# Kernel optimization log

Hardware: AMD Instinct MI355X
Metric: run time of the kernel (lower is better)

## Reference

```python
import jax, jax.numpy as jnp
import numpy as np

B, N, E = 2, 50000, 800000
IN_CH, SP_CH, OUT_CH, EDGE_CH = 64, 16, 32, 1


def _xavier(k, shape):
    scale = (2.0 / (shape[0] + shape[1])) ** 0.5
    return jax.random.normal(k, shape, dtype=jnp.float32) * scale


def setup_inputs() -> dict:
    key = jax.random.key(0)
    ks = jax.random.split(key, 20)
    return {
        "X": jax.random.normal(ks[0], (B, N, IN_CH), dtype=jnp.float32),
        "edge_index0": jax.random.randint(ks[1], (2, E), 0, N),
        "edge_index1": jax.random.randint(ks[2], (2, E), 0, N),
        "edge_weight0": jax.random.uniform(ks[3], (E, EDGE_CH), dtype=jnp.float32),
        "edge_weight1": jax.random.uniform(ks[4], (E, EDGE_CH), dtype=jnp.float32),
        "res_n_id0": jnp.arange(N),
        "res_n_id1": jnp.arange(N),
        # conv1 params (in=IN_CH, out=SP_CH)
        "value1": _xavier(ks[5], (IN_CH, SP_CH)),
        "key1": _xavier(ks[6], (SP_CH, SP_CH)),
        "query1": _xavier(ks[7], (SP_CH, SP_CH)),
        "we1": _xavier(ks[8], (EDGE_CH, SP_CH)),
        "att_w1": _xavier(ks[9], (3 * SP_CH, 1)),
        "att_b1": jnp.zeros((1,), jnp.float32),
        "cat_w1": _xavier(ks[10], (2 * SP_CH, SP_CH)),
        "cat_b1": jnp.zeros((SP_CH,), jnp.float32),
        # conv2 params (in=SP_CH, out=OUT_CH)
        "value2": _xavier(ks[11], (SP_CH, OUT_CH)),
        "key2": _xavier(ks[12], (OUT_CH, OUT_CH)),
        "query2": _xavier(ks[13], (OUT_CH, OUT_CH)),
        "we2": _xavier(ks[14], (EDGE_CH, OUT_CH)),
        "att_w2": _xavier(ks[15], (3 * OUT_CH, 1)),
        "att_b2": jnp.zeros((1,), jnp.float32),
        "cat_w2": _xavier(ks[16], (2 * OUT_CH, OUT_CH)),
        "cat_b2": jnp.zeros((OUT_CH,), jnp.float32),
    }


def _egnn_conv(Xs, Xd, ei, ef, value, key_w, query_w, we, att_w, att_b, cat_w, cat_b):
    # Xs: [B,Ns,Cin] source nodes, Xd: [B,Nd,Cin] dest nodes, ei: [2,E], ef: [E,edge_ch]
    xs = Xs @ value                       # [B,Ns,C]
    xd = Xd @ value                       # [B,Nd,C]
    e = ef @ we                           # [E,C]
    xj = xs[:, ei[0]]                     # [B,E,C] source gather
    xi = xd[:, ei[1]]                     # [B,E,C] dest gather
    q = xj @ query_w                      # note: original code names are swapped; kept faithful
    k = xi @ key_w
    att_in = jnp.concatenate([k, q, jnp.broadcast_to(e, q.shape)], axis=-1)  # [B,E,3C]
    att = jax.nn.sigmoid(att_in @ att_w + att_b)      # [B,E,1]
    msg = att * xj * jax.nn.sigmoid(e)                # [B,E,C]
    aggr = jnp.zeros(xd.shape, xd.dtype).at[:, ei[1]].add(msg)  # scatter-add over dest
    upd = jnp.concatenate([xd, aggr], axis=-1) @ cat_w + cat_b  # [B,Nd,C]
    return xd + jax.nn.relu(upd)


def reference(X, edge_index0, edge_index1, edge_weight0, edge_weight1,
              res_n_id0, res_n_id1,
              value1, key1, query1, we1, att_w1, att_b1, cat_w1, cat_b1,
              value2, key2, query2, we2, att_w2, att_b2, cat_w2, cat_b2):
    X1 = _egnn_conv(X, X[:, res_n_id0], edge_index0, edge_weight0,
                    value1, key1, query1, we1, att_w1, att_b1, cat_w1, cat_b1)
    X1 = jax.nn.leaky_relu(X1)  # negative_slope 0.01, matches torch default
    X2 = _egnn_conv(X1, X1[:, res_n_id1], edge_index1, edge_weight1,
                    value2, key2, query2, we2, att_w2, att_b2, cat_w2, cat_b2)
    return X2
```

## Files before the change

kernel.cpp:

```cpp
#include <hip/hip_runtime.h>
#include <hip/hip_fp16.h>

#define BB   2
#define NN   50000
#define EE   800000
#define INCH 64
#define C1   16
#define C2   32
#define NB   (BB*NN)

#define W1S   6
#define W2S   5
#define NBK1  ((NN + 63) >> 6)
#define NBK2  ((NN + 31) >> 5)
#define NBKT  (NBK1 + NBK2)
#define EB    4096
#define TPB   1024
#define NEBLK ((2*EE + EB - 1) / EB)

#define OFF_XS1   0
#define OFF_XS2   (OFF_XS1 + NB*C1/2)
#define OFF_DOTK1 (OFF_XS2 + NB*C2/2)
#define OFF_DOTQ1 (OFF_DOTK1 + NB)
#define OFF_DOTK2 (OFF_DOTQ1 + NB)
#define OFF_DOTQ2 (OFF_DOTK2 + NB)
#define OFF_AG1   (OFF_DOTQ2 + NB)
#define OFF_AG2   (OFF_AG1 + NN*32)
#define OFF_BTOT  (OFF_AG2 + NN*64)
#define OFF_BBASE (OFF_BTOT + NBKT)
#define OFF_START (OFF_BBASE + NBKT)
#define OFF_DEG   (OFF_START + 2*NN)
#define OFF_SC    (OFF_DEG + 2*NN)
#define OFF_RECS2 (OFF_SC + 2)
#define OFF_REGION (OFF_RECS2 + 2*EE*2)
#define OFF_RECS   OFF_REGION
#define OFF_BCNT   (OFF_REGION + 2*EE*2)

__device__ __forceinline__ float sigmoidf(float x) {
    return 1.0f / (1.0f + __expf(-x));
}

__global__ void k_sc(const float* __restrict__ we1, const float* __restrict__ aw1,
                     const float* __restrict__ we2, const float* __restrict__ aw2,
                     float* __restrict__ sc) {
    if (threadIdx.x == 0) {
        float e = 0.f;
        for (int j = 0; j < C1; ++j) e += we1[j] * aw1[2*C1+j];
        sc[0] = e;
    }
    if (threadIdx.x == 1) {
        float e = 0.f;
        for (int j = 0; j < C2; ++j) e += we2[j] * aw2[2*C2+j];
        sc[1] = e;
    }
}

__global__ __launch_bounds__(TPB) void k_cnt(
        const int* __restrict__ ei0, const int* __restrict__ ei1,
        unsigned* __restrict__ blockCnt) {
    __shared__ unsigned h[NBKT];
    int tid = threadIdx.x;
    for (int i = tid; i < NBKT; i += TPB) h[i] = 0u;
    __syncthreads();
    int base = blockIdx.x * EB;
#pragma unroll
    for (int j = 0; j < EB/TPB; ++j) {
        int t = base + j*TPB + tid;
        if (t < 2*EE) {
            int bkt;
            if (t < EE) { int dst = ei0[EE + t];      bkt = dst >> W1S; }
            else        { int dst = ei1[EE + t - EE]; bkt = NBK1 + (dst >> W2S); }
            atomicAdd(&h[bkt], 1u);
        }
    }
    __syncthreads();
    unsigned* o = blockCnt + (size_t)blockIdx.x * NBKT;
    for (int i = tid; i < NBKT; i += TPB) o[i] = h[i];
}

__global__ __launch_bounds__(512) void k_scanBkt(
        unsigned* __restrict__ blockCnt, unsigned* __restrict__ bktTot) {
    __shared__ unsigned s[512];
    int tid = threadIdx.x;
    int bkt = blockIdx.x;
    unsigned v = (tid < NEBLK) ? blockCnt[(size_t)tid * NBKT + bkt] : 0u;
    s[tid] = v;
    __syncthreads();
    for (int o = 1; o < 512; o <<= 1) {
        unsigned t = (tid >= o) ? s[tid - o] : 0u;
        __syncthreads();
        s[tid] += t;
        __syncthreads();
    }
    if (tid < NEBLK) blockCnt[(size_t)tid * NBKT + bkt] = s[tid] - v;
    if (tid == 511) bktTot[bkt] = s[511];
}

__global__ __launch_bounds__(1024) void k_scanTot(
        const unsigned* __restrict__ bktTot, unsigned* __restrict__ bucketBase) {
    __shared__ unsigned s[1024];
    int tid = threadIdx.x;
    int base = tid * 3;
    unsigned a0 = (base + 0 < NBKT) ? bktTot[base + 0] : 0u;
    unsigned a1 = (base + 1 < NBKT) ? bktTot[base + 1] : 0u;
    unsigned a2 = (base + 2 < NBKT) ? bktTot[base + 2] : 0u;
    unsigned l = a0 + a1 + a2;
    s[tid] = l;
    __syncthreads();
    for (int o = 1; o < 1024; o <<= 1) {
        unsigned t = (tid >= o) ? s[tid - o] : 0u;
        __syncthreads();
        s[tid] += t;
        __syncthreads();
    }
    unsigned ex = s[tid] - l;
    if (base + 0 < NBKT) bucketBase[base + 0] = ex;
    if (base + 1 < NBKT) bucketBase[base + 1] = ex + a0;
    if (base + 2 < NBKT) bucketBase[base + 2] = ex + a0 + a1;
}

__global__ __launch_bounds__(TPB) void k_permute(
        const int* __restrict__ ei0, const int* __restrict__ ei1,
        const float* __restrict__ ew0, const float* __restrict__ ew1,
        const unsigned* __restrict__ blockOff, const unsigned* __restrict__ bucketBase,
        uint2* __restrict__ recs) {
    __shared__ unsigned off[NBKT];
    __shared__ unsigned cur[NBKT];
    int tid = threadIdx.x;
    const unsigned* bo = blockOff + (size_t)blockIdx.x * NBKT;
    for (int i = tid; i < NBKT; i += TPB) { off[i] = bo[i] + bucketBase[i]; cur[i] = 0u; }
    __syncthreads();
    int base = blockIdx.x * EB;
#pragma unroll
    for (int j = 0; j < EB/TPB; ++j) {
        int t = base + j*TPB + tid;
        if (t >= 2*EE) break;
        int bkt, dl, src; float ef;
        if (t < EE) {
            int dst = ei0[EE + t];
            bkt = dst >> W1S; dl = dst & 63;
            src = ei0[t]; ef = ew0[t];
        } else {
            int e = t - EE;
            int dst = ei1[EE + e];
            bkt = NBK1 + (dst >> W2S); dl = dst & 31;
            src = ei1[e]; ef = ew1[e];
        }
        unsigned pos = off[bkt] + atomicAdd(&cur[bkt], 1u);
        recs[pos] = make_uint2((unsigned)src | ((unsigned)dl << 16), __float_as_uint(ef));
    }
}

__global__ __launch_bounds__(256) void k_sortb(
        const uint2* __restrict__ recs, const unsigned* __restrict__ bktTot,
        const unsigned* __restrict__ bucketBase,
        uint2* __restrict__ recs2, unsigned* __restrict__ startA,
        unsigned* __restrict__ degA) {
    __shared__ unsigned h[64], sOff[64], cur[64];
    int tid = threadIdx.x;
    int bkt = blockIdx.x;
    int lay1 = (bkt < NBK1) ? 1 : 0;
    int ndl  = lay1 ? 64 : 32;
    int nodeBase = lay1 ? (bkt << W1S) : ((bkt - NBK1) << W2S);
    int layOff   = lay1 ? 0 : NN;
    if (tid < 64) h[tid] = 0u;
    __syncthreads();
    unsigned cnt = bktTot[bkt], base = bucketBase[bkt];
    for (unsigned i = tid; i < cnt; i += 256)
        atomicAdd(&h[recs[base + i].x >> 16], 1u);
    __syncthreads();
    if (tid == 0) {
        unsigned run = 0;
        for (int d = 0; d < ndl; ++d) { sOff[d] = run; run += h[d]; }
    }
    __syncthreads();
    if (tid < ndl) {
        cur[tid] = sOff[tid];
        int node = nodeBase + tid;
        if (node < NN) {
            startA[layOff + node] = base + sOff[tid];
            degA[layOff + node]   = h[tid];
        }
    }
    __syncthreads();
    for (unsigned i = tid; i < cnt; i += 256) {
        uint2 r = recs[base + i];
        unsigned dl  = r.x >> 16;
        unsigned src = r.x & 0xffffu;
        unsigned pos = atomicAdd(&cur[dl], 1u);
        unsigned dst = (unsigned)nodeBase + dl;
        recs2[base + pos] = make_uint2(src | (dst << 16), r.y);
    }
}

__global__ __launch_bounds__(256) void k_value1(
        const float* __restrict__ X, const float* __restrict__ value1,
        const float* __restrict__ key1, const float* __restrict__ query1,
        const float* __restrict__ aw1,
        __half* __restrict__ xs1h, float* __restrict__ dotk1, float* __restrict__ dotq1) {
    __shared__ float W[INCH*C1];
    __shared__ float KV[C1], QV[C1];
    int tid = threadIdx.x;
    for (int i = tid; i < INCH*C1; i += 256) W[i] = value1[i];
    if (tid < C1) {
        float kv = 0.f, qv = 0.f;
#pragma unroll
        for (int j = 0; j < C1; ++j) {
            kv += key1[tid*C1+j]   * aw1[j];
            qv += query1[tid*C1+j] * aw1[C1+j];
        }
        KV[tid] = kv; QV[tid] = qv;
    }
    __syncthreads();
    int bn = blockIdx.x * 256 + tid;
    if (bn >= NB) return;
    int b = (bn >= NN) ? 1 : 0;
    int node = bn - b*NN;
    const float4* Xr = (const float4*)(X + (size_t)bn * INCH);
    float acc[C1];
#pragma unroll
    for (int j = 0; j < C1; ++j) acc[j] = 0.f;
#pragma unroll
    for (int v = 0; v < 16; ++v) {
        float4 p = Xr[v];
        float x4[4] = {p.x, p.y, p.z, p.w};
#pragma unroll
        for (int h = 0; h < 4; ++h) {
            int i = v*4 + h;
            float xv = x4[h];
#pragma unroll
            for (int j = 0; j < C1; ++j) acc[j] += xv * W[i*C1+j];
        }
    }
    float dk = 0.f, dq = 0.f;
#pragma unroll
    for (int j = 0; j < C1; ++j) { dk += acc[j]*KV[j]; dq += acc[j]*QV[j]; }
    __half* o = xs1h + ((size_t)node * C1) * 2 + b;
#pragma unroll
    for (int j = 0; j < C1; ++j) o[2*j] = __float2half_rn(acc[j]);
    dotk1[node*2 + b] = dk; dotq1[node*2 + b] = dq;
}

__global__ __launch_bounds__(256) void k_gath1(
        const uint2* __restrict__ recs2, const float* __restrict__ we,
        const float* __restrict__ ab, const float* __restrict__ sc,
        const uint2* __restrict__ xsh, const float* __restrict__ dotk,
        const float* __restrict__ dotq, uint2* __restrict__ msg) {
    int t = blockIdx.x * 256 + threadIdx.x;
    int p = t >> 3, cp = t & 7;
    uint2 rec = recs2[p];
    int src = rec.x & 0xffff, dst = rec.x >> 16;
    float ef = __uint_as_float(rec.y);
    float se0 = sigmoidf(ef * we[2*cp]);
    float se1 = sigmoidf(ef * we[2*cp+1]);
    float eb  = ef * sc[0] + ab[0];
    float2 dq = *(const float2*)(dotq + src*2);
    float2 dk = *(const float2*)(dotk + dst*2);
    float a0 = sigmoidf(dk.x + dq.x + eb);
    float a1 = sigmoidf(dk.y + dq.y + eb);
    uint2 xr = xsh[(size_t)src*8 + cp];
    float2 f0 = __half22float2(__builtin_bit_cast(__half2, xr.x));
    float2 f1 = __half22float2(__builtin_bit_cast(__half2, xr.y));
    __half2 m0 = __floats2half2_rn(a0*se0*f0.x, a1*se0*f0.y);
    __half2 m1 = __floats2half2_rn(a0*se1*f1.x, a1*se1*f1.y);
    msg[(size_t)p*8 + cp] = make_uint2(__builtin_bit_cast(unsigned, m0),
                                       __builtin_bit_cast(unsigned, m1));
}

__global__ __launch_bounds__(256) void k_red1(
        const unsigned* __restrict__ startA, const unsigned* __restrict__ degA,
        const uint2* __restrict__ msg, float* __restrict__ aggrf) {
    int t = blockIdx.x * 256 + threadIdx.x;
    int node = t >> 3, cp = t & 7;
    if (node >= NN) return;
    unsigned s = startA[node];
    unsigned n = degA[node];
    float a0 = 0.f, a1 = 0.f, a2 = 0.f, a3 = 0.f;
    const uint2* mp = msg + (size_t)s*8 + cp;
    for (unsigned i = 0; i < n; ++i) {
        uint2 v = mp[(size_t)i*8];
        float2 f0 = __half22float2(__builtin_bit_cast(__half2, v.x));
        float2 f1 = __half22float2(__builtin_bit_cast(__half2, v.y));
        a0 += f0.x; a1 += f0.y; a2 += f1.x; a3 += f1.y;
    }
    ((float4*)aggrf)[(size_t)node*8 + cp] = make_float4(a0, a1, a2, a3);
}

__global__ __launch_bounds__(256) void k_update1(
        const float* __restrict__ cat_w, const float* __restrict__ cat_b,
        const float* __restrict__ value2,
        const float* __restrict__ key2, const float* __restrict__ query2,
        const float* __restrict__ aw2,
        const __half* __restrict__ xs1h, const float* __restrict__ aggr1f,
        __half* __restrict__ xs2h, float* __restrict__ dotk2, float* __restrict__ dotq2) {
    __shared__ float CW[2*C1*C1];
    __shared__ float CB[C1];
    __shared__ float V2[C1*C2];
    __shared__ float KV[C2], QV[C2];
    int tid = threadIdx.x;
    for (int i = tid; i < 2*C1*C1; i += 256) CW[i] = cat_w[i];
    for (int i = tid; i < C1*C2;   i += 256) V2[i] = value2[i];
    if (tid < C1) CB[tid] = cat_b[tid];
    if (tid < C2) {
        float kv = 0.f;
#pragma unroll
        for (int j = 0; j < C2; ++j) kv += key2[tid*C2+j] * aw2[j];
        KV[tid] = kv;
    } else if (tid < 2*C2) {
        int c = tid - C2;
        float qv = 0.f;
#pragma unroll
        for (int j = 0; j < C2; ++j) qv += query2[c*C2+j] * aw2[C2+j];
        QV[c] = qv;
    }
    __syncthreads();
    int bn = blockIdx.x * 256 + tid;
    if (bn >= NB) return;
    int b = (bn >= NN) ? 1 : 0;
    int node = bn - b*NN;
    const __half* xr = xs1h + ((size_t)node*C1)*2 + b;
    const float* agp = aggr1f + (size_t)node*32;
    float xd[C1], ag[C1];
#pragma unroll
    for (int i = 0; i < C1; ++i) xd[i] = __half2float(xr[2*i]);
#pragma unroll
    for (int i = 0; i < C1; ++i) ag[i] = agp[(i>>1)*4 + (i&1)*2 + b];
    float x1[C1];
#pragma unroll
    for (int j = 0; j < C1; ++j) {
        float u = CB[j];
#pragma unroll
        for (int i = 0; i < C1; ++i) {
            u += xd[i] * CW[i*C1 + j];
            u += ag[i] * CW[(C1+i)*C1 + j];
        }
        float o = xd[j] + fmaxf(u, 0.f);
        x1[j] = (o > 0.f) ? o : 0.01f * o;
    }
    float o2[C2];
#pragma unroll
    for (int k = 0; k < C2; ++k) o2[k] = 0.f;
#pragma unroll
    for (int j = 0; j < C1; ++j) {
        float xv = x1[j];
#pragma unroll
        for (int k = 0; k < C2; ++k) o2[k] += xv * V2[j*C2 + k];
    }
    float dk = 0.f, dq = 0.f;
#pragma unroll
    for (int k = 0; k < C2; ++k) { dk += o2[k]*KV[k]; dq += o2[k]*QV[k]; }
    __half* o = xs2h + ((size_t)node*C2)*2 + b;
#pragma unroll
    for (int k = 0; k < C2; ++k) o[2*k] = __float2half_rn(o2[k]);
    dotk2[node*2 + b] = dk; dotq2[node*2 + b] = dq;
}

__global__ __launch_bounds__(256) void k_aggr2f(
        const uint2* __restrict__ recs2, const float* __restrict__ we,
        const float* __restrict__ ab, const float* __restrict__ sc,
        const uint2* __restrict__ xsh, const float* __restrict__ dotk,
        const float* __restrict__ dotq,
        const unsigned* __restrict__ startA, const unsigned* __restrict__ degA,
        float* __restrict__ aggrf) {
    int t = blockIdx.x * 256 + threadIdx.x;
    int node = t >> 4, cp = t & 15;
    if (node >= NN) return;
    unsigned s = startA[NN + node];
    unsigned n = degA[NN + node];
    float w0 = we[2*cp], w1 = we[2*cp+1];
    float ec = sc[1], bias = ab[0];
    float2 dk = *(const float2*)(dotk + node*2);
    float a0 = 0.f, a1 = 0.f, a2 = 0.f, a3 = 0.f;
    int src_n = 0; float ef_n = 0.f; float2 dq_n = make_float2(0.f, 0.f);
    uint2 xr_n = make_uint2(0u, 0u);
    if (n > 0) {
        uint2 r = recs2[s];
        src_n = r.x & 0xffff; ef_n = __uint_as_float(r.y);
        dq_n = *(const float2*)(dotq + src_n*2);
        xr_n = xsh[(size_t)src_n*16 + cp];
    }
    for (unsigned i = 0; i < n; ++i) {
        float ef = ef_n; float2 dq = dq_n; uint2 xr = xr_n;
        if (i + 1 < n) {
            uint2 r = recs2[s + i + 1];
            src_n = r.x & 0xffff; ef_n = __uint_as_float(r.y);
            dq_n = *(const float2*)(dotq + src_n*2);
            xr_n = xsh[(size_t)src_n*16 + cp];
        }
        float se0 = sigmoidf(ef * w0);
        float se1 = sigmoidf(ef * w1);
        float eb  = ef * ec + bias;
        float p0 = sigmoidf(dk.x + dq.x + eb);
        float p1 = sigmoidf(dk.y + dq.y + eb);
        float2 f0 = __half22float2(__builtin_bit_cast(__half2, xr.x));
        float2 f1 = __half22float2(__builtin_bit_cast(__half2, xr.y));
        a0 += p0 * se0 * f0.x;
        a1 += p1 * se0 * f0.y;
        a2 += p0 * se1 * f1.x;
        a3 += p1 * se1 * f1.y;
    }
    ((float4*)aggrf)[(size_t)node*16 + cp] = make_float4(a0, a1, a2, a3);
}

__global__ __launch_bounds__(256) void k_update2(
        const float* __restrict__ cat_w, const float* __restrict__ cat_b,
        const __half* __restrict__ xs2h, const float* __restrict__ aggr2f,
        float* __restrict__ out) {
    __shared__ float CW[2*C2*C2];
    __shared__ float CB[C2];
    int tid = threadIdx.x;
    for (int i = tid; i < 2*C2*C2; i += 256) CW[i] = cat_w[i];
    if (tid < C2) CB[tid] = cat_b[tid];
    __syncthreads();
    int bn = blockIdx.x * 256 + tid;
    if (bn >= NB) return;
    int b = (bn >= NN) ? 1 : 0;
    int node = bn - b*NN;
    const __half* xr = xs2h + ((size_t)node*C2)*2 + b;
    const float* agp = aggr2f + (size_t)node*64;
    float xd[C2], ag[C2];
#pragma unroll
    for (int i = 0; i < C2; ++i) xd[i] = __half2float(xr[2*i]);
#pragma unroll
    for (int i = 0; i < C2; ++i) ag[i] = agp[(i>>1)*4 + (i&1)*2 + b];
    float o[C2];
#pragma unroll
    for (int k = 0; k < C2; ++k) {
        float u = CB[k];
#pragma unroll
        for (int i = 0; i < C2; ++i) {
            u += xd[i] * CW[i*C2 + k];
            u += ag[i] * CW[(C2+i)*C2 + k];
        }
        o[k] = xd[k] + fmaxf(u, 0.f);
    }
    float4* dst = (float4*)(out + (size_t)bn * C2);
#pragma unroll
    for (int v = 0; v < 8; ++v)
        dst[v] = make_float4(o[4*v], o[4*v+1], o[4*v+2], o[4*v+3]);
}

extern "C" void kernel_launch(void* const* d_in, const int* in_sizes, int n_in,
                              void* d_out, int out_size, void* d_ws, size_t ws_size,
                              hipStream_t stream) {
    const float* X      = (const float*)d_in[0];
    const int*   ei0    = (const int*)d_in[1];
    const int*   ei1    = (const int*)d_in[2];
    const float* ew0    = (const float*)d_in[3];
    const float* ew1    = (const float*)d_in[4];
    const float* value1 = (const float*)d_in[7];
    const float* key1   = (const float*)d_in[8];
    const float* query1 = (const float*)d_in[9];
    const float* we1    = (const float*)d_in[10];
    const float* aw1    = (const float*)d_in[11];
    const float* ab1    = (const float*)d_in[12];
    const float* cw1    = (const float*)d_in[13];
    const float* cb1    = (const float*)d_in[14];
    const float* value2 = (const float*)d_in[15];
    const float* key2   = (const float*)d_in[16];
    const float* query2 = (const float*)d_in[17];
    const float* we2    = (const float*)d_in[18];
    const float* aw2    = (const float*)d_in[19];
    const float* ab2    = (const float*)d_in[20];
    const float* cw2    = (const float*)d_in[21];
    const float* cb2    = (const float*)d_in[22];
    float* ws  = (float*)d_ws;
    float* out = (float*)d_out;

    __half* xs1h = (__half*)(ws + OFF_XS1);
    __half* xs2h = (__half*)(ws + OFF_XS2);
    float* aggr1f = ws + OFF_AG1;
    float* aggr2f = ws + OFF_AG2;
    unsigned* blockCnt   = (unsigned*)(ws + OFF_BCNT);
    unsigned* bktTot     = (unsigned*)(ws + OFF_BTOT);
    unsigned* bucketBase = (unsigned*)(ws + OFF_BBASE);
    unsigned* startA     = (unsigned*)(ws + OFF_START);
    unsigned* degA       = (unsigned*)(ws + OFF_DEG);
    uint2*    recs2      = (uint2*)(ws + OFF_RECS2);
    uint2*    recs       = (uint2*)(ws + OFF_RECS);
    uint2*    msg        = (uint2*)(ws + OFF_REGION);

    k_sc<<<1, 64, 0, stream>>>(we1, aw1, we2, aw2, ws + OFF_SC);

    k_value1<<<(NB+255)/256, 256, 0, stream>>>(X, value1, key1, query1, aw1,
                                               xs1h, ws + OFF_DOTK1, ws + OFF_DOTQ1);

    k_cnt<<<NEBLK, TPB, 0, stream>>>(ei0, ei1, blockCnt);
    k_scanBkt<<<NBKT, 512, 0, stream>>>(blockCnt, bktTot);
    k_scanTot<<<1, 1024, 0, stream>>>(bktTot, bucketBase);
    k_permute<<<NEBLK, TPB, 0, stream>>>(ei0, ei1, ew0, ew1,
                                         blockCnt, bucketBase, recs);
    k_sortb<<<NBKT, 256, 0, stream>>>(recs, bktTot, bucketBase,
                                      recs2, startA, degA);

    k_gath1<<<(EE*8)/256, 256, 0, stream>>>(recs2, we1, ab1, ws + OFF_SC,
                                            (const uint2*)xs1h,
                                            ws + OFF_DOTK1, ws + OFF_DOTQ1, msg);
    k_red1<<<(NN*8+255)/256, 256, 0, stream>>>(startA, degA, msg, aggr1f);
    k_update1<<<(NB+255)/256, 256, 0, stream>>>(cw1, cb1, value2, key2, query2, aw2,
                                                xs1h, aggr1f,
                                                xs2h, ws + OFF_DOTK2, ws + OFF_DOTQ2);

    k_aggr2f<<<(NN*16+255)/256, 256, 0, stream>>>(recs2, we2, ab2, ws + OFF_SC,
                                                  (const uint2*)xs2h,
                                                  ws + OFF_DOTK2, ws + OFF_DOTQ2,
                                                  startA, degA, aggr2f);
    k_update2<<<(NB+255)/256, 256, 0, stream>>>(cw2, cb2, xs2h, aggr2f, out);
}
```

Measured before the change: 333.3 us.

## Precompute per-edge attention records and fuse gather into CSR aggregation

Adds a per-edge prep kernel that computes both batch attention sigmoids once per edge and packs them with the source index and a half-precision edge feature into an 8-byte record. Layer 1 drops its materialized per-edge message buffer: the aggregation kernel now gathers source features and applies the edge sigmoid inside its CSR loop. Layer 2 reuses the same prep, so attention is computed once per edge rather than once per channel lane. The sigmoid now uses a hardware reciprocal, and storing the edge feature and attention in fp16 lowers precision.

```diff
diff --git a/kernel.cpp b/kernel.cpp
--- a/kernel.cpp
+++ b/kernel.cpp
@@ -35,9 +35,10 @@
 #define OFF_REGION (OFF_RECS2 + 2*EE*2)
 #define OFF_RECS   OFF_REGION
 #define OFF_BCNT   (OFF_REGION + 2*EE*2)
+#define OFF_PREC   OFF_REGION
 
 __device__ __forceinline__ float sigmoidf(float x) {
-    return 1.0f / (1.0f + __expf(-x));
+    return __builtin_amdgcn_rcpf(1.0f + __expf(-x));
 }
 
 __global__ void k_sc(const float* __restrict__ we1, const float* __restrict__ aw1,
@@ -241,47 +242,59 @@
     dotk1[node*2 + b] = dk; dotq1[node*2 + b] = dq;
 }
 
-__global__ __launch_bounds__(256) void k_gath1(
-        const uint2* __restrict__ recs2, const float* __restrict__ we,
-        const float* __restrict__ ab, const float* __restrict__ sc,
-        const uint2* __restrict__ xsh, const float* __restrict__ dotk,
-        const float* __restrict__ dotq, uint2* __restrict__ msg) {
-    int t = blockIdx.x * 256 + threadIdx.x;
-    int p = t >> 3, cp = t & 7;
-    uint2 rec = recs2[p];
-    int src = rec.x & 0xffff, dst = rec.x >> 16;
-    float ef = __uint_as_float(rec.y);
-    float se0 = sigmoidf(ef * we[2*cp]);
-    float se1 = sigmoidf(ef * we[2*cp+1]);
-    float eb  = ef * sc[0] + ab[0];
+__global__ __launch_bounds__(256) void k_prep(
+        const uint2* __restrict__ recs2seg, const float* __restrict__ dotk,
+        const float* __restrict__ dotq, const float* __restrict__ ab,
+        const float* __restrict__ sc, int scIdx, uint2* __restrict__ prec) {
+    int e = blockIdx.x * 256 + threadIdx.x;
+    uint2 r = recs2seg[e];
+    int src = r.x & 0xffff, dst = r.x >> 16;
+    float ef = __uint_as_float(r.y);
+    float eb = ef * sc[scIdx] + ab[0];
+    float2 dk = *(const float2*)(dotk + dst*2);
     float2 dq = *(const float2*)(dotq + src*2);
-    float2 dk = *(const float2*)(dotk + dst*2);
-    float a0 = sigmoidf(dk.x + dq.x + eb);
-    float a1 = sigmoidf(dk.y + dq.y + eb);
-    uint2 xr = xsh[(size_t)src*8 + cp];
-    float2 f0 = __half22float2(__builtin_bit_cast(__half2, xr.x));
-    float2 f1 = __half22float2(__builtin_bit_cast(__half2, xr.y));
-    __half2 m0 = __floats2half2_rn(a0*se0*f0.x, a1*se0*f0.y);
-    __half2 m1 = __floats2half2_rn(a0*se1*f1.x, a1*se1*f1.y);
-    msg[(size_t)p*8 + cp] = make_uint2(__builtin_bit_cast(unsigned, m0),
-                                       __builtin_bit_cast(unsigned, m1));
-}
-
-__global__ __launch_bounds__(256) void k_red1(
+    float p0 = sigmoidf(dk.x + dq.x + eb);
+    float p1 = sigmoidf(dk.y + dq.y + eb);
+    unsigned pu = __builtin_bit_cast(unsigned, __floats2half2_rn(p0, p1));
+    unsigned eu = (unsigned)__half_as_ushort(__float2half_rn(ef));
+    prec[e] = make_uint2((unsigned)src | (pu << 16),
+                         (pu >> 16) | (eu << 16));
+}
+
+__global__ __launch_bounds__(256) void k_aggr1f(
+        const uint2* __restrict__ prec, const float* __restrict__ we,
+        const uint2* __restrict__ xsh,
         const unsigned* __restrict__ startA, const unsigned* __restrict__ degA,
-        const uint2* __restrict__ msg, float* __restrict__ aggrf) {
+        float* __restrict__ aggrf) {
     int t = blockIdx.x * 256 + threadIdx.x;
     int node = t >> 3, cp = t & 7;
     if (node >= NN) return;
     unsigned s = startA[node];
     unsigned n = degA[node];
+    float w0 = we[2*cp], w1 = we[2*cp+1];
     float a0 = 0.f, a1 = 0.f, a2 = 0.f, a3 = 0.f;
-    const uint2* mp = msg + (size_t)s*8 + cp;
+    uint2 r_n = make_uint2(0u, 0u); uint2 xr_n = make_uint2(0u, 0u);
+    if (n > 0) {
+        r_n = prec[s];
+        xr_n = xsh[(size_t)(r_n.x & 0xffff)*8 + cp];
+    }
     for (unsigned i = 0; i < n; ++i) {
-        uint2 v = mp[(size_t)i*8];
-        float2 f0 = __half22float2(__builtin_bit_cast(__half2, v.x));
-        float2 f1 = __half22float2(__builtin_bit_cast(__half2, v.y));
-        a0 += f0.x; a1 += f0.y; a2 += f1.x; a3 += f1.y;
+        uint2 r = r_n; uint2 xr = xr_n;
+        if (i + 1 < n) {
+            r_n = prec[s + i + 1];
+            xr_n = xsh[(size_t)(r_n.x & 0xffff)*8 + cp];
+        }
+        float p0 = __half2float(__ushort_as_half((unsigned short)(r.x >> 16)));
+        float p1 = __half2float(__ushort_as_half((unsigned short)(r.y & 0xffff)));
+        float ef = __half2float(__ushort_as_half((unsigned short)(r.y >> 16)));
+        float se0 = sigmoidf(ef * w0);
+        float se1 = sigmoidf(ef * w1);
+        float2 f0 = __half22float2(__builtin_bit_cast(__half2, xr.x));
+        float2 f1 = __half22float2(__builtin_bit_cast(__half2, xr.y));
+        a0 += p0 * se0 * f0.x;
+        a1 += p1 * se0 * f0.y;
+        a2 += p0 * se1 * f1.x;
+        a3 += p1 * se1 * f1.y;
     }
     ((float4*)aggrf)[(size_t)node*8 + cp] = make_float4(a0, a1, a2, a3);
 }
@@ -356,42 +369,33 @@
 }
 
 __global__ __launch_bounds__(256) void k_aggr2f(
-        const uint2* __restrict__ recs2, const float* __restrict__ we,
-        const float* __restrict__ ab, const float* __restrict__ sc,
-        const uint2* __restrict__ xsh, const float* __restrict__ dotk,
-        const float* __restrict__ dotq,
+        const uint2* __restrict__ prec, const float* __restrict__ we,
+        const uint2* __restrict__ xsh,
         const unsigned* __restrict__ startA, const unsigned* __restrict__ degA,
         float* __restrict__ aggrf) {
     int t = blockIdx.x * 256 + threadIdx.x;
     int node = t >> 4, cp = t & 15;
     if (node >= NN) return;
-    unsigned s = startA[NN + node];
+    unsigned s = startA[NN + node] - EE;
     unsigned n = degA[NN + node];
     float w0 = we[2*cp], w1 = we[2*cp+1];
-    float ec = sc[1], bias = ab[0];
-    float2 dk = *(const float2*)(dotk + node*2);
     float a0 = 0.f, a1 = 0.f, a2 = 0.f, a3 = 0.f;
-    int src_n = 0; float ef_n = 0.f; float2 dq_n = make_float2(0.f, 0.f);
-    uint2 xr_n = make_uint2(0u, 0u);
+    uint2 r_n = make_uint2(0u, 0u); uint2 xr_n = make_uint2(0u, 0u);
     if (n > 0) {
-        uint2 r = recs2[s];
-        src_n = r.x & 0xffff; ef_n = __uint_as_float(r.y);
-        dq_n = *(const float2*)(dotq + src_n*2);
-        xr_n = xsh[(size_t)src_n*16 + cp];
+        r_n = prec[s];
+        xr_n = xsh[(size_t)(r_n.x & 0xffff)*16 + cp];
     }
     for (unsigned i = 0; i < n; ++i) {
-        float ef = ef_n; float2 dq = dq_n; uint2 xr = xr_n;
+        uint2 r = r_n; uint2 xr = xr_n;
         if (i + 1 < n) {
-            uint2 r = recs2[s + i + 1];
-            src_n = r.x & 0xffff; ef_n = __uint_as_float(r.y);
-            dq_n = *(const float2*)(dotq + src_n*2);
-            xr_n = xsh[(size_t)src_n*16 + cp];
-        }
+            r_n = prec[s + i + 1];
+            xr_n = xsh[(size_t)(r_n.x & 0xffff)*16 + cp];
+        }
+        float p0 = __half2float(__ushort_as_half((unsigned short)(r.x >> 16)));
+        float p1 = __half2float(__ushort_as_half((unsigned short)(r.y & 0xffff)));
+        float ef = __half2float(__ushort_as_half((unsigned short)(r.y >> 16)));
         float se0 = sigmoidf(ef * w0);
         float se1 = sigmoidf(ef * w1);
-        float eb  = ef * ec + bias;
-        float p0 = sigmoidf(dk.x + dq.x + eb);
-        float p1 = sigmoidf(dk.y + dq.y + eb);
         float2 f0 = __half22float2(__builtin_bit_cast(__half2, xr.x));
         float2 f1 = __half22float2(__builtin_bit_cast(__half2, xr.y));
         a0 += p0 * se0 * f0.x;
@@ -478,7 +482,7 @@
     unsigned* degA       = (unsigned*)(ws + OFF_DEG);
     uint2*    recs2      = (uint2*)(ws + OFF_RECS2);
     uint2*    recs       = (uint2*)(ws + OFF_RECS);
-    uint2*    msg        = (uint2*)(ws + OFF_REGION);
+    uint2*    prec       = (uint2*)(ws + OFF_PREC);
 
     k_sc<<<1, 64, 0, stream>>>(we1, aw1, we2, aw2, ws + OFF_SC);
 
@@ -493,17 +497,17 @@
     k_sortb<<<NBKT, 256, 0, stream>>>(recs, bktTot, bucketBase,
                                       recs2, startA, degA);
 
-    k_gath1<<<(EE*8)/256, 256, 0, stream>>>(recs2, we1, ab1, ws + OFF_SC,
-                                            (const uint2*)xs1h,
-                                            ws + OFF_DOTK1, ws + OFF_DOTQ1, msg);
-    k_red1<<<(NN*8+255)/256, 256, 0, stream>>>(startA, degA, msg, aggr1f);
+    k_prep<<<EE/256, 256, 0, stream>>>(recs2, ws + OFF_DOTK1, ws + OFF_DOTQ1,
+                                       ab1, ws + OFF_SC, 0, prec);
+    k_aggr1f<<<(NN*8+255)/256, 256, 0, stream>>>(prec, we1, (const uint2*)xs1h,
+                                                 startA, degA, aggr1f);
     k_update1<<<(NB+255)/256, 256, 0, stream>>>(cw1, cb1, value2, key2, query2, aw2,
                                                 xs1h, aggr1f,
                                                 xs2h, ws + OFF_DOTK2, ws + OFF_DOTQ2);
 
-    k_aggr2f<<<(NN*16+255)/256, 256, 0, stream>>>(recs2, we2, ab2, ws + OFF_SC,
-                                                  (const uint2*)xs2h,
-                                                  ws + OFF_DOTK2, ws + OFF_DOTQ2,
+    k_prep<<<EE/256, 256, 0, stream>>>(recs2 + EE, ws + OFF_DOTK2, ws + OFF_DOTQ2,
+                                       ab2, ws + OFF_SC, 1, prec);
+    k_aggr2f<<<(NN*16+255)/256, 256, 0, stream>>>(prec, we2, (const uint2*)xs2h,
                                                   startA, degA, aggr2f);
     k_update2<<<(NB+255)/256, 256, 0, stream>>>(cw2, cb2, xs2h, aggr2f, out);
 }
```

Result: no change. 327.4 us (-1.8%).
